# Optimization experiments

Measured on AMD Instinct MI355X. Metric: run time of the kernel, lower is better.

## Reference

```python
import jax, jax.numpy as jnp
import numpy as np

HIDDEN = 768
MLP_RATIO = 4
HID_F = HIDDEN * MLP_RATIO          # 3072
NUM_EXPERTS = 6
PART = 192                           # part_features
SHARED = HIDDEN - PART               # 576
B, S = 32, 1024


def setup_inputs() -> dict:
    key = jax.random.key(0)
    ks = jax.random.split(key, 8)
    hidden_state = jax.random.normal(ks[0], (B, S, HIDDEN), dtype=jnp.float32)
    indices = jax.random.randint(ks[1], (B,), 0, NUM_EXPERTS, dtype=jnp.int64)
    sc1 = 1.0 / np.sqrt(HIDDEN)
    sc2 = 1.0 / np.sqrt(HID_F)
    W1 = jax.random.normal(ks[2], (HIDDEN, HID_F), dtype=jnp.float32) * sc1
    b1 = jax.random.normal(ks[3], (HID_F,), dtype=jnp.float32) * sc1
    W2 = jax.random.normal(ks[4], (HID_F, SHARED), dtype=jnp.float32) * sc2
    b2 = jax.random.normal(ks[5], (SHARED,), dtype=jnp.float32) * sc2
    We = jax.random.normal(ks[6], (NUM_EXPERTS, HID_F, PART), dtype=jnp.float32) * sc2
    be = jax.random.normal(ks[7], (NUM_EXPERTS, PART), dtype=jnp.float32) * sc2
    return {"hidden_state": hidden_state, "indices": indices,
            "W1": W1, "b1": b1, "W2": W2, "b2": b2, "We": We, "be": be}


def reference(hidden_state, indices, W1, b1, W2, b2, We, be):
    # fc1 + exact GELU (torch ACT2FN['gelu'])
    h = jnp.einsum('bsd,df->bsf', hidden_state, W1) + b1          # [B,S,HID_F]
    h = jax.nn.gelu(h, approximate=False)
    # shared branch
    shared = jnp.einsum('bsf,fo->bso', h, W2) + b2                # [B,S,SHARED]
    # expert branch: indices select exactly one expert per batch element,
    # so the masked sum over all experts equals gathering the routed expert.
    Wsel = We[indices]                                            # [B,HID_F,PART]
    bsel = be[indices]                                            # [B,PART]
    expert = jnp.einsum('bsf,bfp->bsp', h, Wsel) + bsel[:, None, :]
    return jnp.concatenate([shared, expert], axis=-1)             # [B,S,HIDDEN]
```

## Files before the change

### kernel.cpp

```cpp
#include <hip/hip_runtime.h>
#include <hip/hip_bf16.h>
#include <cstdint>
#include <cstddef>

#define HIDDEN   768
#define HID_F    3072
#define PART     192
#define SHARED_F 576
#define NEXP     6
#define BATCH    32
#define SEQ      1024
#define M_TOK    (BATCH * SEQ)

typedef __bf16 bf16;
typedef __attribute__((ext_vector_type(8))) __bf16 bf16x8;
typedef __attribute__((ext_vector_type(4))) __bf16 bf16x4;
typedef __attribute__((ext_vector_type(4))) float  f32x4;

__device__ __forceinline__ void gl2lds16(const void* g, void* l) {
    __builtin_amdgcn_global_load_lds(
        (const __attribute__((address_space(1))) void*)g,
        (__attribute__((address_space(3))) void*)l,
        16, 0, 0);
}

__device__ __forceinline__ f32x4 mfma16(bf16x8 a, bf16x8 b, f32x4 c) {
    return __builtin_amdgcn_mfma_f32_16x16x32_bf16(a, b, c, 0, 0, 0);
}

#define CFENCE() asm volatile("" ::: "memory")
__device__ __forceinline__ void barrier_raw() {
    CFENCE();
    __builtin_amdgcn_s_barrier();
    CFENCE();
}

__device__ __forceinline__ float gelu_fast(float x) {
    float xs = x * 0.70710678118654752f;
    float ax = __builtin_fabsf(xs);
    float t  = __builtin_amdgcn_rcpf(1.0f + 0.3275911f * ax);
    float p  = t * (0.254829592f +
               t * (-0.284496736f +
               t * (1.421413741f +
               t * (-1.453152027f +
               t * 1.061405429f))));
    float e  = __expf(-xs * xs);
    float er = 1.0f - p * e;
    er = (xs < 0.0f) ? -er : er;
    return 0.5f * x * (1.0f + er);
}

__global__ __launch_bounds__(256) void cvt_f32_bf16(
        const float4* __restrict__ src, bf16x4* __restrict__ dst, int n4) {
    int i      = blockIdx.x * 256 + threadIdx.x;
    int stride = gridDim.x * 256;
    for (; i < n4; i += stride) {
        float4 v = src[i];
        bf16x4 o = { (__bf16)v.x, (__bf16)v.y, (__bf16)v.z, (__bf16)v.w };
        dst[i] = o;
    }
}

__global__ __launch_bounds__(256) void transpose_cvt(
        const float* __restrict__ src, bf16* __restrict__ dst, int K, int N) {
    __shared__ float t[32][33];
    const int n0 = blockIdx.x * 32, k0 = blockIdx.y * 32;
    const int tx = threadIdx.x & 31, ty = threadIdx.x >> 5;
#pragma unroll
    for (int p = 0; p < 4; ++p) {
        int r = ty + p * 8;
        t[r][tx] = src[(size_t)(k0 + r) * N + n0 + tx];
    }
    __syncthreads();
#pragma unroll
    for (int p = 0; p < 4; ++p) {
        int rn = ty + p * 8;
        dst[(size_t)(n0 + rn) * K + k0 + tx] = (bf16)t[tx][rn];
    }
}

__global__ __launch_bounds__(256) void build_wcat(
        const float* __restrict__ W2, const float* __restrict__ We,
        bf16* __restrict__ Wcat) {
    __shared__ float t[32][33];
    const int e  = blockIdx.z;
    const int n0 = blockIdx.x * 32;
    const int k0 = blockIdx.y * 32;
    const int tx = threadIdx.x & 31, ty = threadIdx.x >> 5;
    const float* src;
    int ld, c;
    if (n0 < SHARED_F) { src = W2; ld = SHARED_F; c = n0 + tx; }
    else { src = We + (size_t)e * HID_F * PART; ld = PART; c = n0 + tx - SHARED_F; }
#pragma unroll
    for (int p = 0; p < 4; ++p) {
        int r = ty + p * 8;
        t[r][tx] = src[(size_t)(k0 + r) * ld + c];
    }
    __syncthreads();
    bf16* dst = Wcat + (size_t)e * HIDDEN * HID_F;
#pragma unroll
    for (int p = 0; p < 4; ++p) {
        int rn = ty + p * 8;
        dst[(size_t)(n0 + rn) * HID_F + k0 + tx] = (bf16)t[tx][rn];
    }
}


#define STAGE_A(kt, hm, bb) do {                                          \
    const bf16* g_ = gA + (size_t)((hm) * 128) * LDA + (kt) * 64;         \
    bf16* l_ = lA + ((bb) * 2 + (hm)) * 8192;                             \
    gl2lds16(g_, l_);                                                     \
    gl2lds16(g_ + (size_t)64 * LDA, l_ + 4096);                           \
} while (0)

#define STAGE_B(kt, hm, bb) do {                                          \
    const bf16* g_ = gB + (size_t)((hm) * 128) * LDB + (kt) * 64;         \
    bf16* l_ = lB + ((bb) * 2 + (hm)) * 8192;                             \
    gl2lds16(g_, l_);                                                     \
    gl2lds16(g_ + (size_t)64 * LDB, l_ + 4096);                           \
} while (0)

#define RD_A(dst, qm, bb) do {                                            \
    const bf16* ab_ = fA + ((bb) * 2 + (qm)) * 8192;                      \
    _Pragma("unroll")                                                     \
    for (int mi = 0; mi < 4; ++mi) {                                      \
        dst[mi][0] = *(const bf16x8*)(ab_ + mi * 1024 + pca0);            \
        dst[mi][1] = *(const bf16x8*)(ab_ + mi * 1024 + pca1);            \
    }                                                                     \
} while (0)

#define RD_B(dst, qn, bb) do {                                            \
    const bf16* bb_ = fB + ((bb) * 2 + (qn)) * 8192;                      \
    _Pragma("unroll")                                                     \
    for (int nj = 0; nj < 2; ++nj) {                                      \
        dst[nj][0] = *(const bf16x8*)(bb_ + nj * 1024 + pcb0);            \
        dst[nj][1] = *(const bf16x8*)(bb_ + nj * 1024 + pcb1);            \
    }                                                                     \
} while (0)

#define MFMA16(A_, B_, qm, qn) do {                                       \
    __builtin_amdgcn_s_setprio(1);                                        \
    _Pragma("unroll")                                                     \
    for (int mi = 0; mi < 4; ++mi)                                        \
        _Pragma("unroll")                                                 \
        for (int nj = 0; nj < 2; ++nj) {                                  \
            acc[(qm)*4+mi][(qn)*2+nj] =                                   \
                mfma16(A_[mi][0], B_[nj][0], acc[(qm)*4+mi][(qn)*2+nj]);  \
            acc[(qm)*4+mi][(qn)*2+nj] =                                   \
                mfma16(A_[mi][1], B_[nj][1], acc[(qm)*4+mi][(qn)*2+nj]);  \
        }                                                                 \
    __builtin_amdgcn_s_setprio(0);                                        \
} while (0)

#define TILE(t, b, bo) do {                                               \
    const int tb1_ = ((t) + 1 < NT) ? (t) + 1 : (t) - 1;                  \
    const int ta2_ = ((t) + 2 < NT) ? (t) + 2 : (t);                      \
     \
    asm volatile("s_waitcnt vmcnt(4)" ::: "memory");                      \
    barrier_raw();                                                        \
    RD_B(bfr1, 1, b);                                                     \
    STAGE_B(tb1_, 1, bo);                                                 \
    MFMA16(afr0, bfr0, 0, 0);                                             \
     \
    RD_A(afr1, 1, b);                                                     \
    STAGE_A(tb1_, 1, bo);                                                 \
    MFMA16(afr0, bfr1, 0, 1);                                             \
     \
    STAGE_A(ta2_, 0, b);                                                  \
    MFMA16(afr1, bfr0, 1, 0);                                             \
     \
    asm volatile("s_waitcnt vmcnt(6)" ::: "memory");                      \
    barrier_raw();                                                        \
    RD_A(afr0, 0, bo);                                                    \
    RD_B(bfr0, 0, bo);                                                    \
    STAGE_B(ta2_, 0, b);                                                  \
    MFMA16(afr1, bfr1, 1, 1);                                             \
} while (0)

template<bool IS_FC1>
__global__ __launch_bounds__(512, 2) void fc_8ph(
        const bf16*  __restrict__ A,
        const bf16*  __restrict__ Bmat,
        const float* __restrict__ bias1,
        const float* __restrict__ bias2,
        const int*   __restrict__ idx,
        void*        __restrict__ Outv) {
    constexpr int LDA     = IS_FC1 ? HIDDEN : HID_F;
    constexpr int LDB     = LDA;
    constexpr int NT      = LDA / 64;
    constexpr int NTILE_N = IS_FC1 ? (HID_F / 256) : (HIDDEN / 256);
    constexpr int LDOUT   = IS_FC1 ? HID_F : HIDDEN;

    __shared__ alignas(16) bf16 Abuf[2 * 2 * 128 * 64];
    __shared__ alignas(16) bf16 Bbuf[2 * 2 * 128 * 64];

    const int tid  = threadIdx.x;
    const int wave = tid >> 6, lane = tid & 63;
    const int wm = wave >> 2, wn = wave & 3;
    const int lrow = lane & 15, lk8 = (lane >> 4) & 3;

    const int L   = blockIdx.x;
    const int xcd = L & 7;
    const int j   = L >> 3;
    const int jm  = j / NTILE_N;
    const int mt  = xcd * 16 + jm;
    const int nt  = j - jm * NTILE_N;
    const int m0  = mt * 256;
    const int n0  = nt * 256;

    const bf16* Bt;
    int e = 0;
    if constexpr (IS_FC1) {
        Bt = Bmat;
    } else {
        e = idx[mt >> 2];
        e = e < 0 ? 0 : (e > NEXP - 1 ? NEXP - 1 : e);
        Bt = Bmat + (size_t)e * HIDDEN * HID_F;
    }

    const int srow = tid >> 3;
    const int lch  = (tid & 7) ^ (srow & 7);
    const bf16* gA = A  + (size_t)(m0 + srow) * LDA + lch * 8;
    const bf16* gB = Bt + (size_t)(n0 + srow) * LDB + lch * 8;
    bf16* lA = Abuf + wave * 512;
    bf16* lB = Bbuf + wave * 512;

    const int rA = wm * 64 + lrow;
    const int rB = wn * 32 + lrow;
    const int pca0 = ((0 + lk8) ^ (rA & 7)) * 8;
    const int pca1 = ((4 + lk8) ^ (rA & 7)) * 8;
    const int pcb0 = ((0 + lk8) ^ (rB & 7)) * 8;
    const int pcb1 = ((4 + lk8) ^ (rB & 7)) * 8;
    const bf16* fA = Abuf + rA * 64;
    const bf16* fB = Bbuf + rB * 64;

    f32x4 acc[8][4] = {};
    bf16x8 afr0[4][2], afr1[4][2], bfr0[2][2], bfr1[2][2];

    STAGE_A(0, 0, 0); STAGE_B(0, 0, 0);
    STAGE_B(0, 1, 0); STAGE_A(0, 1, 0);
    STAGE_A(1, 0, 1); STAGE_B(1, 0, 1);
    asm volatile("s_waitcnt vmcnt(8)" ::: "memory");
    barrier_raw();
    RD_A(afr0, 0, 0);
    RD_B(bfr0, 0, 0);

#pragma unroll 1
    for (int t = 0; t < NT; t += 2) {
        TILE(t,     0, 1);
        TILE(t + 1, 1, 0);
    }

    float bv[4];
#pragma unroll
    for (int nj2 = 0; nj2 < 4; ++nj2) {
        const int col = n0 + (nj2 >> 1) * 128 + wn * 32 + (nj2 & 1) * 16 + lrow;
        if constexpr (IS_FC1) {
            bv[nj2] = bias1[col];
        } else {
            bv[nj2] = (col < SHARED_F) ? bias1[col]
                                       : bias2[e * PART + col - SHARED_F];
        }
    }
#pragma unroll
    for (int mi2 = 0; mi2 < 8; ++mi2) {
        const int row0 = m0 + (mi2 >> 2) * 128 + wm * 64 + (mi2 & 3) * 16 + lk8 * 4;
#pragma unroll
        for (int nj2 = 0; nj2 < 4; ++nj2) {
            const int col = n0 + (nj2 >> 1) * 128 + wn * 32 + (nj2 & 1) * 16 + lrow;
            if constexpr (IS_FC1) {
                bf16* o = (bf16*)Outv;
#pragma unroll
                for (int r = 0; r < 4; ++r)
                    o[(size_t)(row0 + r) * LDOUT + col] =
                        (bf16)gelu_fast(acc[mi2][nj2][r] + bv[nj2]);
            } else {
                float* o = (float*)Outv;
#pragma unroll
                for (int r = 0; r < 4; ++r)
                    o[(size_t)(row0 + r) * LDOUT + col] =
                        acc[mi2][nj2][r] + bv[nj2];
            }
        }
    }
}

extern "C" void kernel_launch(void* const* d_in, const int* in_sizes, int n_in,
                              void* d_out, int out_size, void* d_ws, size_t ws_size,
                              hipStream_t stream) {
    const float* hidden = (const float*)d_in[0];
    const int*   idx    = (const int*)d_in[1];
    const float* W1     = (const float*)d_in[2];
    const float* b1     = (const float*)d_in[3];
    const float* W2     = (const float*)d_in[4];
    const float* b2     = (const float*)d_in[5];
    const float* We     = (const float*)d_in[6];
    const float* be     = (const float*)d_in[7];
    float* out = (float*)d_out;

    char* ws = (char*)d_ws;
    bf16* hb   = (bf16*)(ws);
    bf16* h    = (bf16*)(ws + 50331648);
    bf16* W1t  = (bf16*)(ws + 251658240);
    bf16* Wcat = (bf16*)(ws + 256376832);

    cvt_f32_bf16<<<4096, 256, 0, stream>>>(
        (const float4*)hidden, (bf16x4*)hb, (M_TOK * HIDDEN) / 4);
    transpose_cvt<<<dim3(HID_F / 32, HIDDEN / 32), 256, 0, stream>>>(
        W1, W1t, HIDDEN, HID_F);
    build_wcat<<<dim3(HIDDEN / 32, HID_F / 32, NEXP), 256, 0, stream>>>(
        W2, We, Wcat);

    fc_8ph<true><<<(M_TOK / 256) * (HID_F / 256), 512, 0, stream>>>(
        hb, W1t, b1, nullptr, nullptr, h);

    fc_8ph<false><<<(M_TOK / 256) * (HIDDEN / 256), 512, 0, stream>>>(
        h, Wcat, b2, be, idx, out);
}
```

Before: 555.6 us.

## Restructure 8-phase GEMM pipeline with per-phase barriers and reordered staging

```diff
diff --git a/kernel.cpp b/kernel.cpp
--- a/kernel.cpp
+++ b/kernel.cpp
@@ -152,29 +152,44 @@
     __builtin_amdgcn_s_setprio(0);                                        \
 } while (0)
 
+#define WAIT_LGKM0() do {                                                 \
+    asm volatile("s_waitcnt lgkmcnt(0)" ::: "memory");                    \
+    __builtin_amdgcn_sched_barrier(0);                                    \
+} while (0)
+
 #define TILE(t, b, bo) do {                                               \
-    const int tb1_ = ((t) + 1 < NT) ? (t) + 1 : (t) - 1;                  \
-    const int ta2_ = ((t) + 2 < NT) ? (t) + 2 : (t);                      \
-     \
-    asm volatile("s_waitcnt vmcnt(4)" ::: "memory");                      \
-    barrier_raw();                                                        \
+    const int tp1_ = ((t) + 1 < NT) ? (t) + 1 : (t) - 1;                  \
+    const int tp2_ = ((t) + 2 < NT) ? (t) + 2 : (t);                      \
+    \
+    RD_A(afr0, 0, b);                                                     \
+    RD_B(bfr0, 0, b);                                                     \
+    STAGE_A(tp1_, 1, bo);                                                 \
+    asm volatile("s_waitcnt lgkmcnt(8)" ::: "memory");                    \
+    barrier_raw();                                                        \
+    WAIT_LGKM0();                                                         \
+    MFMA16(afr0, bfr0, 0, 0);                                             \
+    barrier_raw();                                                        \
+    \
     RD_B(bfr1, 1, b);                                                     \
-    STAGE_B(tb1_, 1, bo);                                                 \
-    MFMA16(afr0, bfr0, 0, 0);                                             \
-     \
+    STAGE_A(tp2_, 0, b);                                                  \
+    barrier_raw();                                                        \
+    WAIT_LGKM0();                                                         \
+    MFMA16(afr0, bfr1, 0, 1);                                             \
+    barrier_raw();                                                        \
+    \
     RD_A(afr1, 1, b);                                                     \
-    STAGE_A(tb1_, 1, bo);                                                 \
-    MFMA16(afr0, bfr1, 0, 1);                                             \
-     \
-    STAGE_A(ta2_, 0, b);                                                  \
+    STAGE_B(tp2_, 0, b);                                                  \
+    barrier_raw();                                                        \
+    WAIT_LGKM0();                                                         \
     MFMA16(afr1, bfr0, 1, 0);                                             \
-     \
+    barrier_raw();                                                        \
+    \
+    STAGE_B(tp2_, 1, b);                                                  \
     asm volatile("s_waitcnt vmcnt(6)" ::: "memory");                      \
     barrier_raw();                                                        \
-    RD_A(afr0, 0, bo);                                                    \
-    RD_B(bfr0, 0, bo);                                                    \
-    STAGE_B(ta2_, 0, b);                                                  \
+    __builtin_amdgcn_sched_barrier(0);                                    \
     MFMA16(afr1, bfr1, 1, 1);                                             \
+    barrier_raw();                                                        \
 } while (0)
 
 template<bool IS_FC1>
@@ -237,13 +252,10 @@
     f32x4 acc[8][4] = {};
     bf16x8 afr0[4][2], afr1[4][2], bfr0[2][2], bfr1[2][2];
 
-    STAGE_A(0, 0, 0); STAGE_B(0, 0, 0);
-    STAGE_B(0, 1, 0); STAGE_A(0, 1, 0);
-    STAGE_A(1, 0, 1); STAGE_B(1, 0, 1);
-    asm volatile("s_waitcnt vmcnt(8)" ::: "memory");
+    STAGE_A(0, 0, 0); STAGE_B(0, 0, 0); STAGE_B(0, 1, 0); STAGE_A(0, 1, 0);
+    STAGE_A(1, 0, 1); STAGE_B(1, 0, 1); STAGE_B(1, 1, 1);
+    asm volatile("s_waitcnt vmcnt(6)" ::: "memory");
     barrier_raw();
-    RD_A(afr0, 0, 0);
-    RD_B(bfr0, 0, 0);
 
 #pragma unroll 1
     for (int t = 0; t < NT; t += 2) {
```

New measurement: 593.4 us. +6.8%, slower.

## Use 256x192 output tiles in FC2 kernel to fill all CUs

Applied to the files above, without the earlier changes.

```diff
diff --git a/kernel.cpp b/kernel.cpp
--- a/kernel.cpp
+++ b/kernel.cpp
@@ -120,6 +120,10 @@
     gl2lds16(g_ + (size_t)64 * LDB, l_ + 4096);                           \
 } while (0)
 
+#define STAGE_B3(kt, nj, bb)                                              \
+    gl2lds16(gB + (size_t)((nj) * 64) * LDB + (kt) * 64,                  \
+             lB + ((bb) * 3 + (nj)) * 4096)
+
 #define RD_A(dst, qm, bb) do {                                            \
     const bf16* ab_ = fA + ((bb) * 2 + (qm)) * 8192;                      \
     _Pragma("unroll")                                                     \
@@ -136,6 +140,12 @@
         dst[nj][0] = *(const bf16x8*)(bb_ + nj * 1024 + pcb0);            \
         dst[nj][1] = *(const bf16x8*)(bb_ + nj * 1024 + pcb1);            \
     }                                                                     \
+} while (0)
+
+#define RD_B3(dst, nj, bb) do {                                           \
+    const bf16* b3_ = fB + ((bb) * 3 + (nj)) * 4096;                      \
+    dst[0] = *(const bf16x8*)(b3_ + pcb0);                                \
+    dst[1] = *(const bf16x8*)(b3_ + pcb1);                                \
 } while (0)
 
 #define MFMA16(A_, B_, qm, qn) do {                                       \
@@ -149,6 +159,18 @@
             acc[(qm)*4+mi][(qn)*2+nj] =                                   \
                 mfma16(A_[mi][1], B_[nj][1], acc[(qm)*4+mi][(qn)*2+nj]);  \
         }                                                                 \
+    __builtin_amdgcn_s_setprio(0);                                        \
+} while (0)
+
+#define MFMA8(A_, B_, qm, nj) do {                                        \
+    __builtin_amdgcn_s_setprio(1);                                        \
+    _Pragma("unroll")                                                     \
+    for (int mi = 0; mi < 4; ++mi) {                                      \
+        acc[(qm)*4+mi][nj] =                                              \
+            mfma16(A_[mi][0], B_[0], acc[(qm)*4+mi][nj]);                 \
+        acc[(qm)*4+mi][nj] =                                              \
+            mfma16(A_[mi][1], B_[1], acc[(qm)*4+mi][nj]);                 \
+    }                                                                     \
     __builtin_amdgcn_s_setprio(0);                                        \
 } while (0)
 
@@ -177,19 +199,15 @@
     MFMA16(afr1, bfr1, 1, 1);                                             \
 } while (0)
 
-template<bool IS_FC1>
-__global__ __launch_bounds__(512, 2) void fc_8ph(
+__global__ __launch_bounds__(512, 2) void fc1_8ph(
         const bf16*  __restrict__ A,
         const bf16*  __restrict__ Bmat,
         const float* __restrict__ bias1,
-        const float* __restrict__ bias2,
-        const int*   __restrict__ idx,
-        void*        __restrict__ Outv) {
-    constexpr int LDA     = IS_FC1 ? HIDDEN : HID_F;
-    constexpr int LDB     = LDA;
-    constexpr int NT      = LDA / 64;
-    constexpr int NTILE_N = IS_FC1 ? (HID_F / 256) : (HIDDEN / 256);
-    constexpr int LDOUT   = IS_FC1 ? HID_F : HIDDEN;
+        bf16*        __restrict__ Out) {
+    constexpr int LDA = HIDDEN, LDB = HIDDEN;
+    constexpr int NT  = LDA / 64;
+    constexpr int NTILE_N = HID_F / 256;
+    constexpr int LDOUT   = HID_F;
 
     __shared__ alignas(16) bf16 Abuf[2 * 2 * 128 * 64];
     __shared__ alignas(16) bf16 Bbuf[2 * 2 * 128 * 64];
@@ -208,20 +226,10 @@
     const int m0  = mt * 256;
     const int n0  = nt * 256;
 
-    const bf16* Bt;
-    int e = 0;
-    if constexpr (IS_FC1) {
-        Bt = Bmat;
-    } else {
-        e = idx[mt >> 2];
-        e = e < 0 ? 0 : (e > NEXP - 1 ? NEXP - 1 : e);
-        Bt = Bmat + (size_t)e * HIDDEN * HID_F;
-    }
-
     const int srow = tid >> 3;
     const int lch  = (tid & 7) ^ (srow & 7);
-    const bf16* gA = A  + (size_t)(m0 + srow) * LDA + lch * 8;
-    const bf16* gB = Bt + (size_t)(n0 + srow) * LDB + lch * 8;
+    const bf16* gA = A    + (size_t)(m0 + srow) * LDA + lch * 8;
+    const bf16* gB = Bmat + (size_t)(n0 + srow) * LDB + lch * 8;
     bf16* lA = Abuf + wave * 512;
     bf16* lB = Bbuf + wave * 512;
 
@@ -240,7 +248,7 @@
     STAGE_A(0, 0, 0); STAGE_B(0, 0, 0);
     STAGE_B(0, 1, 0); STAGE_A(0, 1, 0);
     STAGE_A(1, 0, 1); STAGE_B(1, 0, 1);
-    asm volatile("s_waitcnt vmcnt(8)" ::: "memory");
+    asm volatile("s_waitcnt vmcnt(4)" ::: "memory");
     barrier_raw();
     RD_A(afr0, 0, 0);
     RD_B(bfr0, 0, 0);
@@ -255,12 +263,7 @@
 #pragma unroll
     for (int nj2 = 0; nj2 < 4; ++nj2) {
         const int col = n0 + (nj2 >> 1) * 128 + wn * 32 + (nj2 & 1) * 16 + lrow;
-        if constexpr (IS_FC1) {
-            bv[nj2] = bias1[col];
-        } else {
-            bv[nj2] = (col < SHARED_F) ? bias1[col]
-                                       : bias2[e * PART + col - SHARED_F];
-        }
+        bv[nj2] = bias1[col];
     }
 #pragma unroll
     for (int mi2 = 0; mi2 < 8; ++mi2) {
@@ -268,19 +271,123 @@
 #pragma unroll
         for (int nj2 = 0; nj2 < 4; ++nj2) {
             const int col = n0 + (nj2 >> 1) * 128 + wn * 32 + (nj2 & 1) * 16 + lrow;
-            if constexpr (IS_FC1) {
-                bf16* o = (bf16*)Outv;
-#pragma unroll
-                for (int r = 0; r < 4; ++r)
-                    o[(size_t)(row0 + r) * LDOUT + col] =
-                        (bf16)gelu_fast(acc[mi2][nj2][r] + bv[nj2]);
-            } else {
-                float* o = (float*)Outv;
-#pragma unroll
-                for (int r = 0; r < 4; ++r)
-                    o[(size_t)(row0 + r) * LDOUT + col] =
-                        acc[mi2][nj2][r] + bv[nj2];
-            }
+#pragma unroll
+            for (int r = 0; r < 4; ++r)
+                Out[(size_t)(row0 + r) * LDOUT + col] =
+                    (bf16)gelu_fast(acc[mi2][nj2][r] + bv[nj2]);
+        }
+    }
+}
+
+__global__ __launch_bounds__(512, 2) void fc2_moe192(
+        const bf16*  __restrict__ A,
+        const bf16*  __restrict__ Bmat,
+        const float* __restrict__ b2,
+        const float* __restrict__ be,
+        const int*   __restrict__ idx,
+        float*       __restrict__ Out) {
+    constexpr int LDA = HID_F, LDB = HID_F;
+    constexpr int NT  = LDA / 64;
+    constexpr int NTILE_N = HIDDEN / 192;
+    constexpr int LDOUT   = HIDDEN;
+
+    __shared__ alignas(16) bf16 Abuf[2 * 2 * 128 * 64];
+    __shared__ alignas(16) bf16 Bbuf[2 * 3 * 64 * 64];
+
+    const int tid  = threadIdx.x;
+    const int wave = tid >> 6, lane = tid & 63;
+    const int wm = wave >> 2, wn = wave & 3;
+    const int lrow = lane & 15, lk8 = (lane >> 4) & 3;
+
+    const int L   = blockIdx.x;
+    const int xcd = L & 7;
+    const int j   = L >> 3;
+    const int jm  = j >> 2;
+    const int mt  = xcd * 16 + jm;
+    const int nt  = j & 3;
+    const int m0  = mt * 256;
+    const int n0  = nt * 192;
+
+    int e = idx[mt >> 2];
+    e = e < 0 ? 0 : (e > NEXP - 1 ? NEXP - 1 : e);
+    const bf16* Bt = Bmat + (size_t)e * HIDDEN * HID_F;
+
+    const int srow = tid >> 3;
+    const int lch  = (tid & 7) ^ (srow & 7);
+    const bf16* gA = A  + (size_t)(m0 + srow) * LDA + lch * 8;
+    const bf16* gB = Bt + (size_t)(n0 + srow) * LDB + lch * 8;
+    bf16* lA = Abuf + wave * 512;
+    bf16* lB = Bbuf + wave * 512;
+
+    const int rA  = wm * 64 + lrow;
+    const int rBc = wn * 16 + lrow;
+    const int pca0 = ((0 + lk8) ^ (rA & 7)) * 8;
+    const int pca1 = ((4 + lk8) ^ (rA & 7)) * 8;
+    const int pcb0 = ((0 + lk8) ^ (rBc & 7)) * 8;
+    const int pcb1 = ((4 + lk8) ^ (rBc & 7)) * 8;
+    const bf16* fA = Abuf + rA * 64;
+    const bf16* fB = Bbuf + rBc * 64;
+
+    f32x4 acc[8][3] = {};
+    bf16x8 afr0[4][2], afr1[4][2];
+    bf16x8 bfrA[2], bfrB[2], bfrC[2];
+
+    STAGE_A(0, 0, 0);
+    STAGE_B3(0, 0, 0); STAGE_B3(0, 1, 0); STAGE_B3(0, 2, 0);
+    STAGE_A(0, 1, 0);
+    STAGE_A(1, 0, 1);
+    STAGE_B3(1, 0, 1); STAGE_B3(1, 1, 1);
+    asm volatile("s_waitcnt vmcnt(4)" ::: "memory");
+    barrier_raw();
+    RD_A(afr0, 0, 0);
+    RD_B3(bfrA, 0, 0);
+    RD_B3(bfrB, 1, 0);
+
+#pragma unroll 1
+    for (int t = 0; t < NT; t += 2) {
+#pragma unroll
+        for (int u = 0; u < 2; ++u) {
+            const int tt = t + u;
+            const int b  = u, bo = u ^ 1;
+            const int tp1 = (tt + 1 < NT) ? tt + 1 : tt - 1;
+            const int tp2 = (tt + 2 < NT) ? tt + 2 : tt;
+            STAGE_A(tp1, 1, bo);
+            asm volatile("s_waitcnt vmcnt(4)" ::: "memory");
+            barrier_raw();
+            RD_B3(bfrC, 2, b);
+            MFMA8(afr0, bfrA, 0, 0);
+            MFMA8(afr0, bfrB, 0, 1);
+            STAGE_B3(tp1, 2, bo);
+            RD_A(afr1, 1, b);
+            MFMA8(afr0, bfrC, 0, 2);
+            STAGE_A(tp2, 0, b);
+            MFMA8(afr1, bfrA, 1, 0);
+            MFMA8(afr1, bfrB, 1, 1);
+            STAGE_B3(tp2, 0, b); STAGE_B3(tp2, 1, b);
+            asm volatile("s_waitcnt vmcnt(4)" ::: "memory");
+            barrier_raw();
+            RD_A(afr0, 0, bo);
+            RD_B3(bfrA, 0, bo);
+            RD_B3(bfrB, 1, bo);
+            MFMA8(afr1, bfrC, 1, 2);
+        }
+    }
+
+    float bv[3];
+#pragma unroll
+    for (int nj = 0; nj < 3; ++nj) {
+        const int col = n0 + nj * 64 + wn * 16 + lrow;
+        bv[nj] = (col < SHARED_F) ? b2[col] : be[e * PART + col - SHARED_F];
+    }
+#pragma unroll
+    for (int mi2 = 0; mi2 < 8; ++mi2) {
+        const int row0 = m0 + (mi2 >> 2) * 128 + wm * 64 + (mi2 & 3) * 16 + lk8 * 4;
+#pragma unroll
+        for (int nj = 0; nj < 3; ++nj) {
+            const int col = n0 + nj * 64 + wn * 16 + lrow;
+#pragma unroll
+            for (int r = 0; r < 4; ++r)
+                Out[(size_t)(row0 + r) * LDOUT + col] = acc[mi2][nj][r] + bv[nj];
         }
     }
 }
@@ -311,9 +418,9 @@
     build_wcat<<<dim3(HIDDEN / 32, HID_F / 32, NEXP), 256, 0, stream>>>(
         W2, We, Wcat);
 
-    fc_8ph<true><<<(M_TOK / 256) * (HID_F / 256), 512, 0, stream>>>(
-        hb, W1t, b1, nullptr, nullptr, h);
-
-    fc_8ph<false><<<(M_TOK / 256) * (HIDDEN / 256), 512, 0, stream>>>(
+    fc1_8ph<<<(M_TOK / 256) * (HID_F / 256), 512, 0, stream>>>(
+        hb, W1t, b1, h);
+
+    fc2_moe192<<<(M_TOK / 256) * (HIDDEN / 192), 512, 0, stream>>>(
         h, Wcat, b2, be, idx, out);
 }
```

Result: no change. 546.6 us (-1.6%).
